# Performance work log

Hardware: AMD Instinct MI355X
Metric: run time of the kernel (lower is better)

The kernel has to match this reference:

```python
import jax, jax.numpy as jnp
import numpy as np
from jax import lax

B, T, N, C = 32, 32, 64, 64          # batch, window, num_series, inter_dim
GRU_H, QK, HOR = 64, 32, 12          # gru_dim, qk_dim, prediction_horizon
KS = (3, 5, 7)                       # temporal kernel per block (3 + 2*i)


def setup_inputs() -> dict:
    key = jax.random.key(0)
    ks = jax.random.split(key, 32)
    rn = lambda k, shape, s=0.05: jax.random.normal(k, shape, jnp.float32) * s
    inp = {"x": jax.random.normal(ks[0], (B, T, N), jnp.float32)}
    # x_to_inter_dim: Conv1d(1, C, kernel_size=1) == scalar * w + b
    inp["w_x2i"] = rn(ks[1], (C,)); inp["b_x2i"] = rn(ks[2], (C,))
    # latentCorrelation GRU (input_size=1, hidden=GRU_H), gate order r,z,n
    inp["gru_wih"] = rn(ks[3], (3 * GRU_H, 1)); inp["gru_whh"] = rn(ks[4], (3 * GRU_H, GRU_H))
    inp["gru_bih"] = rn(ks[5], (3 * GRU_H,)); inp["gru_bhh"] = rn(ks[6], (3 * GRU_H,))
    inp["wq_w"] = rn(ks[7], (QK, GRU_H)); inp["wq_b"] = rn(ks[8], (QK,))
    inp["wk_w"] = rn(ks[9], (QK, GRU_H)); inp["wk_b"] = rn(ks[10], (QK,))
    # per block: T independent GCNConvs (theta + bias), one temporal Conv1d
    for i, k_ in enumerate(KS):
        inp[f"gcn_w{i}"] = rn(ks[11 + 4 * i], (T, C, C))
        inp[f"gcn_b{i}"] = rn(ks[12 + 4 * i], (T, C))
        inp[f"conv_w{i}"] = rn(ks[13 + 4 * i], (C, C, k_))
        inp[f"conv_b{i}"] = rn(ks[14 + 4 * i], (C,))
    inp["lout_w"] = rn(ks[25], (N * HOR, T * N * C), 0.01)
    inp["lout_b"] = rn(ks[26], (N * HOR,))
    return inp


def _forward(x, w_x2i, b_x2i, gru_wih, gru_whh, gru_bih, gru_bhh,
             wq_w, wq_b, wk_w, wk_b,
             gcn_w0, gcn_b0, conv_w0, conv_b0,
             gcn_w1, gcn_b1, conv_w1, conv_b1,
             gcn_w2, gcn_b2, conv_w2, conv_b2,
             lout_w, lout_b):
    xs = jnp.transpose(x, (1, 0, 2))  # (T, B, N) time-major

    # --- latentCorrelation: one GRU run over all B*N series at once ---
    def gru_step(h, xt):  # h: (B,N,GRU_H), xt: (B,N)
        gi = xt[..., None] * gru_wih[:, 0] + gru_bih           # (B,N,3H)
        gh = h @ gru_whh.T + gru_bhh                           # (B,N,3H)
        r = jax.nn.sigmoid(gi[..., :GRU_H] + gh[..., :GRU_H])
        z = jax.nn.sigmoid(gi[..., GRU_H:2 * GRU_H] + gh[..., GRU_H:2 * GRU_H])
        n = jnp.tanh(gi[..., 2 * GRU_H:] + r * gh[..., 2 * GRU_H:])
        return (1.0 - z) * n + z * h, None

    h0 = jnp.zeros((B, N, GRU_H), x.dtype)
    hT, _ = lax.scan(gru_step, h0, xs)                         # (B,N,GRU_H)
    Q = hT @ wq_w.T + wq_b                                     # (B,N,QK)
    K = hT @ wk_w.T + wk_b
    Wadj = jax.nn.softmax(jnp.einsum('bnq,bmq->bnm', Q, K) / jnp.sqrt(jnp.float32(QK)), axis=2)

    # GCN symmetric norm on the dense complete graph; edge (src=i, tgt=j) has
    # weight Wadj[b,i,j]; degree is per-target (column) sum.
    deg = Wadj.sum(axis=1)                                     # (B,N)
    dinv = jnp.where(deg > 0, 1.0 / jnp.sqrt(deg), 0.0)
    What = dinv[:, :, None] * Wadj * dinv[:, None, :]          # (B,N,N)

    # x_to_inter_dim (1x1 conv) applied per timestep
    feats = xs[..., None] * w_x2i + b_x2i                      # (T,B,N,C)

    for gw, gb, cw, cb, k_ in ((gcn_w0, gcn_b0, conv_w0, conv_b0, 3),
                               (gcn_w1, gcn_b1, conv_w1, conv_b1, 5),
                               (gcn_w2, gcn_b2, conv_w2, conv_b2, 7)):
        xw = jnp.einsum('tbnc,tcd->tbnd', feats, gw)           # per-timestep theta
        agg = jnp.einsum('bij,tbid->tbjd', What, xw) + gb[:, None, None, :]
        seq = jnp.transpose(agg, (1, 2, 3, 0)).reshape(B * N, C, T)
        p = k_ // 2
        conv = lax.conv_general_dilated(seq, cw, (1,), [(p, p)],
                                        dimension_numbers=('NCH', 'OIH', 'NCH'))
        conv = conv + cb[None, :, None]
        conv = jnp.where(conv >= 0, conv, 0.01 * conv)         # LeakyReLU (dropout p=0)
        feats = jnp.transpose(conv.reshape(B, N, C, T), (3, 0, 1, 2))

    # stack(x_list, dim=2).view(B*N, C*T).view(B, -1) -> (B, N*C*T) feature order (n,c,t)
    flat = jnp.transpose(feats, (1, 2, 3, 0)).reshape(B, N * C * T)
    out = flat @ lout_w.T + lout_b                             # (B, N*HOR)
    return out.reshape(B, HOR, N)


def reference(x, w_x2i, b_x2i, gru_wih, gru_whh, gru_bih, gru_bhh,
              wq_w, wq_b, wk_w, wk_b,
              gcn_w0, gcn_b0, conv_w0, conv_b0,
              gcn_w1, gcn_b1, conv_w1, conv_b1,
              gcn_w2, gcn_b2, conv_w2, conv_b2,
              lout_w, lout_b):
    return _forward(x, w_x2i, b_x2i, gru_wih, gru_whh, gru_bih, gru_bhh,
                    wq_w, wq_b, wk_w, wk_b,
                    gcn_w0, gcn_b0, conv_w0, conv_b0,
                    gcn_w1, gcn_b1, conv_w1, conv_b1,
                    gcn_w2, gcn_b2, conv_w2, conv_b2,
                    lout_w, lout_b)
```

## Files before the change

### kernel.cpp

```cpp
#include <hip/hip_runtime.h>
#include <hip/hip_bf16.h>

#define BB 32
#define TT 32
#define NN 64
#define CC 64
#define HH 64
#define QKD 32
#define HOR 12
#define OUTD (NN*HOR)
#define KFLAT (NN*CC*TT)

typedef __attribute__((ext_vector_type(4))) float f32x4;
typedef __attribute__((ext_vector_type(8))) short s16x8;

static __device__ __forceinline__ unsigned short f2bf(float f) {
    unsigned u = __float_as_uint(f);
    unsigned r = (u + 0x7FFFu + ((u >> 16) & 1u)) >> 16;
    return (unsigned short)r;
}
static __device__ __forceinline__ float bf2f(unsigned short h) {
    return __uint_as_float(((unsigned)h) << 16);
}
static __device__ __forceinline__ void split8(const float* f, uint4& hi, uint4& lo) {
    unsigned hh[8], ll[8];
    #pragma unroll
    for (int i = 0; i < 8; ++i) {
        unsigned short h = f2bf(f[i]);
        float hf = bf2f(h);
        hh[i] = h;
        ll[i] = f2bf(f[i] - hf);
    }
    hi = make_uint4(hh[0] | (hh[1] << 16), hh[2] | (hh[3] << 16),
                    hh[4] | (hh[5] << 16), hh[6] | (hh[7] << 16));
    lo = make_uint4(ll[0] | (ll[1] << 16), ll[2] | (ll[3] << 16),
                    ll[4] | (ll[5] << 16), ll[6] | (ll[7] << 16));
}
static __device__ __forceinline__ void gl2lds16(const void* gsrc, void* ldst) {
    __builtin_amdgcn_global_load_lds(
        (const __attribute__((address_space(1))) unsigned int*)gsrc,
        (__attribute__((address_space(3))) unsigned int*)ldst, 16, 0, 0);
}

__global__ __launch_bounds__(256) void gru_kernel(
    const float* __restrict__ x, const float* __restrict__ wih,
    const float* __restrict__ whh, const float* __restrict__ bih,
    const float* __restrict__ bhh, float* __restrict__ hT)
{
    __shared__ float Wt[64][193];
    __shared__ float hbuf[4][64];
    __shared__ float part[4][4][3][64];
    int tid = threadIdx.x;
    for (int idx = tid; idx < 192*64; idx += 256) {
        int g = idx >> 6, k = idx & 63;
        Wt[k][g] = whh[idx];
    }
    int w = tid >> 6;
    int j = tid & 63;
    hbuf[w][j] = 0.0f;
    __syncthreads();
    float Wreg[3][16];
    #pragma unroll
    for (int g = 0; g < 3; ++g)
        #pragma unroll
        for (int kk = 0; kk < 16; ++kk)
            Wreg[g][kk] = Wt[w*16 + kk][g*64 + j];
    int gs0 = blockIdx.x * 4;
    int b = gs0 >> 6, n0 = gs0 & 63;
    float wih_r = wih[j], wih_z = wih[64+j], wih_n = wih[128+j];
    float bi_r = bih[j], bi_z = bih[64+j], bi_n = bih[128+j];
    float bh_r = bhh[j], bh_z = bhh[64+j], bh_n = bhh[128+j];
    float hreg = 0.0f;
    for (int t = 0; t < TT; ++t) {
        float p[3][4];
        #pragma unroll
        for (int g = 0; g < 3; ++g)
            #pragma unroll
            for (int s = 0; s < 4; ++s) p[g][s] = 0.f;
        #pragma unroll
        for (int s = 0; s < 4; ++s) {
            #pragma unroll
            for (int q = 0; q < 4; ++q) {
                const float4 hv = *(const float4*)&hbuf[s][w*16 + q*4];
                #pragma unroll
                for (int g = 0; g < 3; ++g) {
                    p[g][s] += hv.x*Wreg[g][q*4]   + hv.y*Wreg[g][q*4+1]
                             + hv.z*Wreg[g][q*4+2] + hv.w*Wreg[g][q*4+3];
                }
            }
        }
        #pragma unroll
        for (int g = 0; g < 3; ++g)
            #pragma unroll
            for (int s = 0; s < 4; ++s)
                part[w][s][g][j] = p[g][s];
        __syncthreads();
        float gr = bh_r + part[0][w][0][j] + part[1][w][0][j] + part[2][w][0][j] + part[3][w][0][j];
        float gz = bh_z + part[0][w][1][j] + part[1][w][1][j] + part[2][w][1][j] + part[3][w][1][j];
        float gn = bh_n + part[0][w][2][j] + part[1][w][2][j] + part[2][w][2][j] + part[3][w][2][j];
        float xt = x[(b*TT + t)*NN + n0 + w];
        float r = 1.f/(1.f+__expf(-(xt*wih_r + bi_r + gr)));
        float z = 1.f/(1.f+__expf(-(xt*wih_z + bi_z + gz)));
        float nn_ = tanhf(xt*wih_n + bi_n + r*gn);
        float hnew = (1.f - z)*nn_ + z*hreg;
        hreg = hnew;
        hbuf[w][j] = hnew;
        __syncthreads();
    }
    hT[(gs0 + w)*64 + j] = hreg;
}

__global__ __launch_bounds__(256) void attn_kernel(
    const float* __restrict__ hT, const float* __restrict__ wq_w,
    const float* __restrict__ wq_b, const float* __restrict__ wk_w,
    const float* __restrict__ wk_b,
    unsigned short* __restrict__ whT_hi, unsigned short* __restrict__ whT_lo)
{
    __shared__ float hs[64][64];
    __shared__ float Qs[64][33], Ks[64][33];
    __shared__ float S[64][65];
    __shared__ float pd[4][64];
    __shared__ float dinv[64];
    int b = blockIdx.x, tid = threadIdx.x;
    for (int idx = tid; idx < 64*64; idx += 256) hs[idx>>6][idx&63] = hT[b*4096 + idx];
    __syncthreads();
    for (int idx = tid; idx < 64*32; idx += 256) {
        int n_ = idx >> 5, q = idx & 31;
        float accq = wq_b[q], acck = wk_b[q];
        #pragma unroll 8
        for (int h_ = 0; h_ < 64; ++h_) {
            float hv = hs[n_][h_];
            accq += hv * wq_w[q*64 + h_];
            acck += hv * wk_w[q*64 + h_];
        }
        Qs[n_][q] = accq; Ks[n_][q] = acck;
    }
    __syncthreads();
    const float scale = 0.17677669529663687f;
    for (int idx = tid; idx < 64*64; idx += 256) {
        int n_ = idx >> 6, m = idx & 63;
        float acc = 0.f;
        #pragma unroll 8
        for (int q = 0; q < 32; ++q) acc += Qs[n_][q]*Ks[m][q];
        S[n_][m] = acc * scale;
    }
    __syncthreads();
    {
        int r = tid >> 2, q = tid & 3;
        float mx = -1e30f;
        #pragma unroll
        for (int m = 0; m < 16; ++m) mx = fmaxf(mx, S[r][q*16+m]);
        mx = fmaxf(mx, __shfl_xor(mx, 1));
        mx = fmaxf(mx, __shfl_xor(mx, 2));
        float sum = 0.f;
        float e[16];
        #pragma unroll
        for (int m = 0; m < 16; ++m) { e[m] = __expf(S[r][q*16+m]-mx); sum += e[m]; }
        sum += __shfl_xor(sum, 1);
        sum += __shfl_xor(sum, 2);
        float inv = 1.f/sum;
        #pragma unroll
        for (int m = 0; m < 16; ++m) S[r][q*16+m] = e[m]*inv;
    }
    __syncthreads();
    {
        int c = tid & 63, rq = tid >> 6;
        float d = 0.f;
        #pragma unroll
        for (int i = 0; i < 16; ++i) d += S[rq*16 + i][c];
        pd[rq][c] = d;
    }
    __syncthreads();
    if (tid < 64) {
        float d = pd[0][tid]+pd[1][tid]+pd[2][tid]+pd[3][tid];
        dinv[tid] = (d > 0.f) ? 1.0f/sqrtf(d) : 0.f;
    }
    __syncthreads();
    for (int idx = tid; idx < 64*64; idx += 256) {
        int jj = idx >> 6, ii = idx & 63;
        float val = dinv[ii]*S[ii][jj]*dinv[jj];
        unsigned short h = f2bf(val);
        whT_hi[b*4096 + idx] = h;
        whT_lo[b*4096 + idx] = f2bf(val - bf2f(h));
    }
}

__global__ __launch_bounds__(256) void prep_all(
    const float* __restrict__ gw0, const float* __restrict__ wx, const float* __restrict__ bx,
    float* __restrict__ u, float* __restrict__ v,
    const float* __restrict__ gw1, unsigned short* __restrict__ g1h, unsigned short* __restrict__ g1l,
    const float* __restrict__ gw2, unsigned short* __restrict__ g2h, unsigned short* __restrict__ g2l,
    const float* __restrict__ cw1, unsigned short* __restrict__ c1h, unsigned short* __restrict__ c1l,
    const float* __restrict__ cw2, unsigned short* __restrict__ c2h, unsigned short* __restrict__ c2l,
    const float* __restrict__ cw3, unsigned short* __restrict__ c3h, unsigned short* __restrict__ c3l,
    const float* __restrict__ lb, float* __restrict__ out)
{
    int bid = blockIdx.x, tid = threadIdx.x;
    if (bid < 32) {
        __shared__ float pu[4][64], pv[4][64];
        int t = bid, d = tid & 63, cq = tid >> 6;
        float su = 0.f, sv = 0.f;
        for (int c = cq*16; c < cq*16 + 16; ++c) {
            float gv = gw0[t*4096 + c*64 + d];
            su += wx[c]*gv; sv += bx[c]*gv;
        }
        pu[cq][d] = su; pv[cq][d] = sv;
        __syncthreads();
        if (tid < 64) {
            u[t*64 + tid] = pu[0][tid]+pu[1][tid]+pu[2][tid]+pu[3][tid];
            v[t*64 + tid] = pv[0][tid]+pv[1][tid]+pv[2][tid]+pv[3][tid];
        }
    } else if (bid < 96) {
        const float* gw = (bid < 64) ? gw1 : gw2;
        unsigned short* hi = (bid < 64) ? g1h : g2h;
        unsigned short* lo = (bid < 64) ? g1l : g2l;
        int t = (bid < 64) ? bid - 32 : bid - 64;
        for (int idx = tid; idx < 4096; idx += 256) {
            int d = idx >> 6, c = idx & 63;
            float val = gw[t*4096 + c*64 + d];
            unsigned short h = f2bf(val);
            hi[t*4096 + idx] = h;
            lo[t*4096 + idx] = f2bf(val - bf2f(h));
        }
    } else if (bid < 288) {
        const float* cw; unsigned short *hi, *lo; int KW, co;
        if (bid < 160)      { cw = cw1; hi = c1h; lo = c1l; KW = 3; co = bid - 96; }
        else if (bid < 224) { cw = cw2; hi = c2h; lo = c2l; KW = 5; co = bid - 160; }
        else                { cw = cw3; hi = c3h; lo = c3l; KW = 7; co = bid - 224; }
        int K = KW*64;
        for (int idx = tid; idx < K; idx += 256) {
            int ka = idx >> 6, ci = idx & 63;
            float val = cw[(size_t)(co*64 + ci)*KW + ka];
            unsigned short h = f2bf(val);
            hi[(size_t)co*K + idx] = h;
            lo[(size_t)co*K + idx] = f2bf(val - bf2f(h));
        }
    } else {
        int idx = (bid - 288)*256 + tid;
        out[idx] = lb[idx % OUTD];
    }
}

template<bool FIRST>
__global__ __launch_bounds__(256) void gcn_mfma(
    const float* __restrict__ fin,
    const unsigned short* __restrict__ gwT_hi, const unsigned short* __restrict__ gwT_lo,
    const float* __restrict__ u, const float* __restrict__ v,
    const unsigned short* __restrict__ whT_hi, const unsigned short* __restrict__ whT_lo,
    const float* __restrict__ gb, float* __restrict__ o)
{
    __shared__ __align__(16) unsigned short ft_hi[64][64], ft_lo[64][64];
    __shared__ __align__(16) unsigned short xsT_hi[64][64], xsT_lo[64][64];
    __shared__ float x_l[64];
    int tb = blockIdx.x, t = tb >> 5, b = tb & 31;
    int tid = threadIdx.x;
    int w = tid >> 6, l = tid & 63, lm = l & 15, ld = l >> 4;

    if (FIRST) {
        if (tid < 64) x_l[tid] = fin[(b*TT + t)*NN + tid];
        __syncthreads();
        int d = tid >> 2, nq = tid & 3;
        float ud = u[t*64 + d], vd = v[t*64 + d];
        float vals[16];
        #pragma unroll
        for (int i = 0; i < 16; ++i) vals[i] = x_l[nq*16 + i]*ud + vd;
        #pragma unroll
        for (int h = 0; h < 2; ++h) {
            uint4 hi, lo; split8(&vals[h*8], hi, lo);
            int un = (nq*2 + h) ^ (d & 7);
            *(uint4*)&xsT_hi[d][un*8] = hi;
            *(uint4*)&xsT_lo[d][un*8] = lo;
        }
        __syncthreads();
    } else {
        {
            int row = tid >> 2, c0 = (tid & 3) * 16;
            const float* src = fin + (size_t)tb*4096 + row*64 + c0;
            float f8a[8], f8b[8];
            *(float4*)f8a = *(const float4*)src;       *(float4*)(f8a+4) = *(const float4*)(src+4);
            *(float4*)f8b = *(const float4*)(src+8);   *(float4*)(f8b+4) = *(const float4*)(src+12);
            uint4 hi, lo;
            split8(f8a, hi, lo);
            int u0 = ((c0>>3)) ^ (row & 7);
            *(uint4*)&ft_hi[row][u0*8] = hi; *(uint4*)&ft_lo[row][u0*8] = lo;
            split8(f8b, hi, lo);
            int u1 = ((c0>>3)+1) ^ (row & 7);
            *(uint4*)&ft_hi[row][u1*8] = hi; *(uint4*)&ft_lo[row][u1*8] = lo;
        }
        __syncthreads();
        f32x4 acc[4];
        #pragma unroll
        for (int ct = 0; ct < 4; ++ct) acc[ct] = (f32x4){0.f,0.f,0.f,0.f};
        #pragma unroll
        for (int kc = 0; kc < 2; ++kc) {
            int nrow = w*16 + lm;
            int ux = (kc*4 + ld) ^ (nrow & 7);
            s16x8 xh = *(const s16x8*)&ft_hi[nrow][ux*8];
            s16x8 xl = *(const s16x8*)&ft_lo[nrow][ux*8];
            #pragma unroll
            for (int ct = 0; ct < 4; ++ct) {
                int drow = ct*16 + lm;
                s16x8 yh = *(const s16x8*)&gwT_hi[t*4096 + drow*64 + kc*32 + ld*8];
                s16x8 yl = *(const s16x8*)&gwT_lo[t*4096 + drow*64 + kc*32 + ld*8];
                acc[ct] = __builtin_amdgcn_mfma_f32_16x16x32_bf16(xh, yh, acc[ct], 0, 0, 0);
                acc[ct] = __builtin_amdgcn_mfma_f32_16x16x32_bf16(xh, yl, acc[ct], 0, 0, 0);
                acc[ct] = __builtin_amdgcn_mfma_f32_16x16x32_bf16(xl, yh, acc[ct], 0, 0, 0);
            }
        }
        #pragma unroll
        for (int ct = 0; ct < 4; ++ct) {
            int d = ct*16 + lm;
            int n0 = w*16 + ld*4;
            unsigned short hh[4], llo[4];
            #pragma unroll
            for (int r = 0; r < 4; ++r) {
                float val = acc[ct][r];
                unsigned short h = f2bf(val);
                hh[r] = h; llo[r] = f2bf(val - bf2f(h));
            }
            int un = (n0 >> 3) ^ (d & 7);
            int base = d*64 + un*8 + (n0 & 7);
            *(uint2*)&xsT_hi[0][0 + base] = make_uint2(hh[0]|(hh[1]<<16), hh[2]|(hh[3]<<16));
            *(uint2*)&xsT_lo[0][0 + base] = make_uint2(llo[0]|(llo[1]<<16), llo[2]|(llo[3]<<16));
        }
        __syncthreads();
    }

    f32x4 acc2[4];
    #pragma unroll
    for (int ct = 0; ct < 4; ++ct) acc2[ct] = (f32x4){0.f,0.f,0.f,0.f};
    #pragma unroll
    for (int kc = 0; kc < 2; ++kc) {
        int jrow = w*16 + lm;
        s16x8 wh = *(const s16x8*)&whT_hi[b*4096 + jrow*64 + kc*32 + ld*8];
        s16x8 wl = *(const s16x8*)&whT_lo[b*4096 + jrow*64 + kc*32 + ld*8];
        #pragma unroll
        for (int ct = 0; ct < 4; ++ct) {
            int drow = ct*16 + lm;
            int uy = (kc*4 + ld) ^ (drow & 7);
            s16x8 yh = *(const s16x8*)&xsT_hi[drow][uy*8];
            s16x8 yl = *(const s16x8*)&xsT_lo[drow][uy*8];
            acc2[ct] = __builtin_amdgcn_mfma_f32_16x16x32_bf16(wh, yh, acc2[ct], 0, 0, 0);
            acc2[ct] = __builtin_amdgcn_mfma_f32_16x16x32_bf16(wh, yl, acc2[ct], 0, 0, 0);
            acc2[ct] = __builtin_amdgcn_mfma_f32_16x16x32_bf16(wl, yh, acc2[ct], 0, 0, 0);
        }
    }
    float* oo = o + (size_t)tb*4096;
    #pragma unroll
    for (int ct = 0; ct < 4; ++ct) {
        int d = ct*16 + lm;
        float bias = gb[t*64 + d];
        #pragma unroll
        for (int r = 0; r < 4; ++r) {
            int jj = w*16 + ld*4 + r;
            oo[jj*64 + d] = acc2[ct][r] + bias;
        }
    }
}

template<int KW, bool LAST>
__global__ __launch_bounds__(256) void conv_mfma(float* __restrict__ g,
    const unsigned short* __restrict__ wch, const unsigned short* __restrict__ wcl,
    const float* __restrict__ cb, unsigned short* __restrict__ fo)
{
    constexpr int P = KW/2, K = KW*64, K32 = KW*2;
    __shared__ __align__(16) unsigned short sh[32][64], sl[32][64];
    int bn = blockIdx.x, tid = threadIdx.x;
    {
        int t = tid >> 3, c0 = (tid & 7) * 8;
        const float* src = &g[((size_t)t*2048 + bn)*64 + c0];
        float f8[8];
        *(float4*)f8 = *(const float4*)src;
        *(float4*)(f8+4) = *(const float4*)(src+4);
        uint4 hi, lo; split8(f8, hi, lo);
        int uu = (tid & 7) ^ (t & 7);
        *(uint4*)&sh[t][uu*8] = hi;
        *(uint4*)&sl[t][uu*8] = lo;
    }
    __syncthreads();
    int w = tid >> 6, l = tid & 63, lm = l & 15, ld = l >> 4;
    int co = w*16 + lm;
    f32x4 acc0 = {0.f,0.f,0.f,0.f}, acc1 = {0.f,0.f,0.f,0.f};
    const s16x8 zf = {0,0,0,0,0,0,0,0};
    for (int kc = 0; kc < K32; ++kc) {
        int ka = kc >> 1;
        int ci = (kc & 1)*32 + ld*8;
        s16x8 yh = *(const s16x8*)&wch[(size_t)co*K + kc*32 + ld*8];
        s16x8 yl = *(const s16x8*)&wcl[(size_t)co*K + kc*32 + ld*8];
        #pragma unroll
        for (int Mt = 0; Mt < 2; ++Mt) {
            int ts = Mt*16 + lm + ka - P;
            bool ok = ((unsigned)ts) < 32u;
            int tc = ok ? ts : 0;
            int ua = (ci >> 3) ^ (tc & 7);
            s16x8 xh = *(const s16x8*)&sh[tc][ua*8];
            s16x8 xl = *(const s16x8*)&sl[tc][ua*8];
            if (!ok) { xh = zf; xl = zf; }
            f32x4& a = Mt ? acc1 : acc0;
            a = __builtin_amdgcn_mfma_f32_16x16x32_bf16(xh, yh, a, 0, 0, 0);
            a = __builtin_amdgcn_mfma_f32_16x16x32_bf16(xh, yl, a, 0, 0, 0);
            a = __builtin_amdgcn_mfma_f32_16x16x32_bf16(xl, yh, a, 0, 0, 0);
        }
    }
    float bias = cb[co];
    if (LAST) {
        int b = bn >> 6, n = bn & 63;
        unsigned short* ob = fo + (size_t)b*KFLAT + n*2048 + co*32;
        #pragma unroll
        for (int Mt = 0; Mt < 2; ++Mt) {
            const f32x4& a = Mt ? acc1 : acc0;
            unsigned short hv[4];
            #pragma unroll
            for (int r = 0; r < 4; ++r) {
                float val = a[r] + bias;
                val = (val >= 0.f) ? val : 0.01f*val;
                hv[r] = f2bf(val);
            }
            *(uint2*)&ob[Mt*16 + ld*4] = make_uint2(hv[0]|(hv[1]<<16), hv[2]|(hv[3]<<16));
        }
    } else {
        #pragma unroll
        for (int Mt = 0; Mt < 2; ++Mt) {
            const f32x4& a = Mt ? acc1 : acc0;
            #pragma unroll
            for (int r = 0; r < 4; ++r) {
                int t = Mt*16 + ld*4 + r;
                float val = a[r] + bias;
                val = (val >= 0.f) ? val : 0.01f*val;
                g[((size_t)t*2048 + bn)*64 + co] = val;
            }
        }
    }
}

__global__ __launch_bounds__(256) void gemm_mfma(const unsigned short* __restrict__ flat,
                                                 const float* __restrict__ W,
                                                 float* __restrict__ out)
{
    __shared__ __align__(16) float Wl[2][64][64];
    __shared__ __align__(16) unsigned short Al[2][32][64];
    const int tid = threadIdx.x;
    const int w = tid >> 6, l = tid & 63;
    const int og = blockIdx.x >> 6;
    const int kc = blockIdx.x & 63;
    const int o_blk = og * 64;
    const int kbase = kc * 2048;

    const int wrow_l = l >> 4;
    const int wu = l & 15;
    size_t w_off[4];
    #pragma unroll
    for (int i = 0; i < 4; ++i) {
        int row = w*16 + i*4 + wrow_l;
        w_off[i] = (size_t)(o_blk + row) * KFLAT + (unsigned)((wu ^ (row & 7)) * 4);
    }
    const int arow = w*8 + (l >> 3);
    const int au = l & 7;
    const size_t a_off0 = (size_t)arow * KFLAT + (unsigned)((au ^ (arow & 7)) * 8);

#define ISSUE_TILE(buf_, s_) { \
    int kwin_ = kbase + (s_)*64; \
    _Pragma("unroll") \
    for (int i_ = 0; i_ < 4; ++i_) \
        gl2lds16(W + w_off[i_] + kwin_, &Wl[buf_][w*16 + i_*4][0]); \
    gl2lds16(flat + a_off0 + kwin_, &Al[buf_][w*8][0]); \
}

    f32x4 acc0 = {0.f,0.f,0.f,0.f}, acc1 = {0.f,0.f,0.f,0.f};
    ISSUE_TILE(0, 0);
    ISSUE_TILE(1, 1);

    const int lmod = l & 15, ldiv = l >> 4, lx = l & 7;
    for (int s = 0; s < 32; ++s) {
        if (s < 31) { asm volatile("s_waitcnt vmcnt(5)" ::: "memory"); }
        else        { asm volatile("s_waitcnt vmcnt(0)" ::: "memory"); }
        __builtin_amdgcn_s_barrier();
        asm volatile("" ::: "memory");
        const int cur = s & 1;
        #pragma unroll
        for (int ksub = 0; ksub < 2; ++ksub) {
            int ju = ksub*8 + ldiv*2;
            const float4 b0 = *(const float4*)&Wl[cur][w*16 + lmod][(ju ^ lx)*4];
            const float4 b1 = *(const float4*)&Wl[cur][w*16 + lmod][((ju+1) ^ lx)*4];
            float bf[8] = {b0.x,b0.y,b0.z,b0.w,b1.x,b1.y,b1.z,b1.w};
            s16x8 bhi, blo;
            #pragma unroll
            for (int i = 0; i < 8; ++i) {
                unsigned short h = f2bf(bf[i]);
                float hf = bf2f(h);
                bhi[i] = (short)h;
                blo[i] = (short)f2bf(bf[i] - hf);
            }
            int jua = ksub*4 + ldiv;
            const s16x8 a0 = *(const s16x8*)&Al[cur][lmod]      [(jua ^ lx)*8];
            const s16x8 a1 = *(const s16x8*)&Al[cur][16 + lmod] [(jua ^ lx)*8];
            acc0 = __builtin_amdgcn_mfma_f32_16x16x32_bf16(a0, bhi, acc0, 0, 0, 0);
            acc0 = __builtin_amdgcn_mfma_f32_16x16x32_bf16(a0, blo, acc0, 0, 0, 0);
            acc1 = __builtin_amdgcn_mfma_f32_16x16x32_bf16(a1, bhi, acc1, 0, 0, 0);
            acc1 = __builtin_amdgcn_mfma_f32_16x16x32_bf16(a1, blo, acc1, 0, 0, 0);
        }
        asm volatile("" ::: "memory");
        __builtin_amdgcn_s_barrier();
        if (s < 30) { ISSUE_TILE(cur, s+2); }
    }
#undef ISSUE_TILE

    const int o_out = o_blk + w*16 + lmod;
    #pragma unroll
    for (int r = 0; r < 4; ++r) {
        int b0_ = ldiv*4 + r;
        atomicAdd(&out[(size_t)b0_*OUTD + o_out], acc0[r]);
        atomicAdd(&out[(size_t)(16 + b0_)*OUTD + o_out], acc1[r]);
    }
}

extern "C" void kernel_launch(void* const* d_in, const int* in_sizes, int n_in,
                              void* d_out, int out_size, void* d_ws, size_t ws_size,
                              hipStream_t stream) {
    (void)in_sizes; (void)n_in; (void)out_size; (void)ws_size;
    const float* x        = (const float*)d_in[0];
    const float* w_x2i    = (const float*)d_in[1];
    const float* b_x2i    = (const float*)d_in[2];
    const float* gru_wih  = (const float*)d_in[3];
    const float* gru_whh  = (const float*)d_in[4];
    const float* gru_bih  = (const float*)d_in[5];
    const float* gru_bhh  = (const float*)d_in[6];
    const float* wq_w     = (const float*)d_in[7];
    const float* wq_b     = (const float*)d_in[8];
    const float* wk_w     = (const float*)d_in[9];
    const float* wk_b     = (const float*)d_in[10];
    const float* gcn_w[3]  = {(const float*)d_in[11], (const float*)d_in[15], (const float*)d_in[19]};
    const float* gcn_b[3]  = {(const float*)d_in[12], (const float*)d_in[16], (const float*)d_in[20]};
    const float* conv_w[3] = {(const float*)d_in[13], (const float*)d_in[17], (const float*)d_in[21]};
    const float* conv_b[3] = {(const float*)d_in[14], (const float*)d_in[18], (const float*)d_in[22]};
    const float* lout_w   = (const float*)d_in[23];
    const float* lout_b   = (const float*)d_in[24];
    float* out = (float*)d_out;
    float* ws  = (float*)d_ws;

    float* hT   = ws;
    float* u    = ws + 131072;
    float* v    = ws + 133120;
    float* bufA = ws + 135168;
    float* bufB = bufA + 4194304;
    unsigned short* usb = (unsigned short*)(ws + 8523776);
    unsigned short* whT_hi  = usb;
    unsigned short* whT_lo  = usb + 131072;
    unsigned short* gwT1_hi = usb + 262144;
    unsigned short* gwT1_lo = usb + 393216;
    unsigned short* gwT2_hi = usb + 524288;
    unsigned short* gwT2_lo = usb + 655360;
    unsigned short* cw1_hi  = usb + 786432;
    unsigned short* cw1_lo  = usb + 798720;
    unsigned short* cw2_hi  = usb + 811008;
    unsigned short* cw2_lo  = usb + 831488;
    unsigned short* cw3_hi  = usb + 851968;
    unsigned short* cw3_lo  = usb + 880640;

    prep_all<<<dim3(384), dim3(256), 0, stream>>>(
        gcn_w[0], w_x2i, b_x2i, u, v,
        gcn_w[1], gwT1_hi, gwT1_lo,
        gcn_w[2], gwT2_hi, gwT2_lo,
        conv_w[0], cw1_hi, cw1_lo,
        conv_w[1], cw2_hi, cw2_lo,
        conv_w[2], cw3_hi, cw3_lo,
        lout_b, out);

    gru_kernel<<<dim3(512), dim3(256), 0, stream>>>(x, gru_wih, gru_whh, gru_bih, gru_bhh, hT);
    attn_kernel<<<dim3(32), dim3(256), 0, stream>>>(hT, wq_w, wq_b, wk_w, wk_b, whT_hi, whT_lo);

    unsigned short* flat16 = (unsigned short*)bufB;
    gcn_mfma<true><<<dim3(1024), dim3(256), 0, stream>>>(x, nullptr, nullptr, u, v,
                                                         whT_hi, whT_lo, gcn_b[0], bufA);
    conv_mfma<3,false><<<dim3(2048), dim3(256), 0, stream>>>(bufA, cw1_hi, cw1_lo, conv_b[0], nullptr);
    gcn_mfma<false><<<dim3(1024), dim3(256), 0, stream>>>(bufA, gwT1_hi, gwT1_lo, u, v,
                                                          whT_hi, whT_lo, gcn_b[1], bufB);
    conv_mfma<5,false><<<dim3(2048), dim3(256), 0, stream>>>(bufB, cw2_hi, cw2_lo, conv_b[1], nullptr);
    gcn_mfma<false><<<dim3(1024), dim3(256), 0, stream>>>(bufB, gwT2_hi, gwT2_lo, u, v,
                                                          whT_hi, whT_lo, gcn_b[2], bufA);
    conv_mfma<7,true><<<dim3(2048), dim3(256), 0, stream>>>(bufA, cw3_hi, cw3_lo, conv_b[2], (unsigned short*)bufB);

    gemm_mfma<<<dim3(768), dim3(256), 0, stream>>>(flat16, lout_w, out);
}
```

Before: 307.8 us.

## Fuse middle stages into persistent kernel with grid barriers; single-bf16 final GEMM

Merges the prep, GRU, attention, GCN and conv kernels into one persistent 512-block kernel that separates stages with software grid barriers, removing per-launch gaps. The final GEMM now uses a triple-buffered load pipeline that issues tile loads before compute, and it drops the low half of the split-bf16 weights, halving its MFMA count. The grid barrier assumes all 512 blocks are co-resident, and deadlocks if they are not. Dropping the low-order weight term lowers the GEMM's accuracy.

```diff
diff --git a/kernel.cpp b/kernel.cpp
--- a/kernel.cpp
+++ b/kernel.cpp
@@ -10,23 +10,25 @@
 #define HOR 12
 #define OUTD (NN*HOR)
 #define KFLAT (NN*CC*TT)
+#define NBLK 512
 
 typedef __attribute__((ext_vector_type(4))) float f32x4;
 typedef __attribute__((ext_vector_type(8))) short s16x8;
-
-static __device__ __forceinline__ unsigned short f2bf(float f) {
+typedef unsigned short ush;
+
+static __device__ __forceinline__ ush f2bf(float f) {
     unsigned u = __float_as_uint(f);
     unsigned r = (u + 0x7FFFu + ((u >> 16) & 1u)) >> 16;
-    return (unsigned short)r;
-}
-static __device__ __forceinline__ float bf2f(unsigned short h) {
+    return (ush)r;
+}
+static __device__ __forceinline__ float bf2f(ush h) {
     return __uint_as_float(((unsigned)h) << 16);
 }
 static __device__ __forceinline__ void split8(const float* f, uint4& hi, uint4& lo) {
     unsigned hh[8], ll[8];
     #pragma unroll
     for (int i = 0; i < 8; ++i) {
-        unsigned short h = f2bf(f[i]);
+        ush h = f2bf(f[i]);
         float hf = bf2f(h);
         hh[i] = h;
         ll[i] = f2bf(f[i] - hf);
@@ -42,219 +44,56 @@
         (__attribute__((address_space(3))) unsigned int*)ldst, 16, 0, 0);
 }
 
-__global__ __launch_bounds__(256) void gru_kernel(
-    const float* __restrict__ x, const float* __restrict__ wih,
-    const float* __restrict__ whh, const float* __restrict__ bih,
-    const float* __restrict__ bhh, float* __restrict__ hT)
+static __device__ __forceinline__ void gridbar(unsigned* bar, int k) {
+    __syncthreads();
+    if (threadIdx.x == 0) {
+        __threadfence();
+        unsigned* cnt = bar + 2*k;
+        unsigned* flg = bar + 2*k + 1;
+        unsigned prev = atomicAdd(cnt, 1u);
+        if (prev == NBLK - 1u) {
+            __threadfence();
+            atomicExch(flg, 1u);
+        } else {
+            while (atomicAdd(flg, 0u) == 0u) __builtin_amdgcn_s_sleep(4);
+        }
+        __threadfence();
+    }
+    __syncthreads();
+}
+
+struct MidP {
+    const float *x, *wih, *whh, *bih, *bhh;
+    float* hT;
+    const float *wq_w, *wq_b, *wk_w, *wk_b;
+    ush *whT_hi, *whT_lo;
+    const float *gw0, *wx, *bx;
+    float *u, *v;
+    const float *gw1; ush *g1h, *g1l;
+    const float *gw2; ush *g2h, *g2l;
+    const float *cw1; ush *c1h, *c1l;
+    const float *cw2; ush *c2h, *c2l;
+    const float *cw3; ush *c3h, *c3l;
+    const float *lb; float* out;
+    const float *gb0, *gb1, *gb2, *cb1, *cb2, *cb3;
+    float *bufA, *bufB; ush* flat16;
+    unsigned* bar;
+};
+
+template<bool FIRST>
+static __device__ void gcn_unit(int tb, const float* fin,
+    const ush* gwT_hi, const ush* gwT_lo, const float* u, const float* v,
+    const ush* whT_hi, const ush* whT_lo, const float* gb, float* o, char* smem)
 {
-    __shared__ float Wt[64][193];
-    __shared__ float hbuf[4][64];
-    __shared__ float part[4][4][3][64];
-    int tid = threadIdx.x;
-    for (int idx = tid; idx < 192*64; idx += 256) {
-        int g = idx >> 6, k = idx & 63;
-        Wt[k][g] = whh[idx];
-    }
-    int w = tid >> 6;
-    int j = tid & 63;
-    hbuf[w][j] = 0.0f;
-    __syncthreads();
-    float Wreg[3][16];
-    #pragma unroll
-    for (int g = 0; g < 3; ++g)
-        #pragma unroll
-        for (int kk = 0; kk < 16; ++kk)
-            Wreg[g][kk] = Wt[w*16 + kk][g*64 + j];
-    int gs0 = blockIdx.x * 4;
-    int b = gs0 >> 6, n0 = gs0 & 63;
-    float wih_r = wih[j], wih_z = wih[64+j], wih_n = wih[128+j];
-    float bi_r = bih[j], bi_z = bih[64+j], bi_n = bih[128+j];
-    float bh_r = bhh[j], bh_z = bhh[64+j], bh_n = bhh[128+j];
-    float hreg = 0.0f;
-    for (int t = 0; t < TT; ++t) {
-        float p[3][4];
-        #pragma unroll
-        for (int g = 0; g < 3; ++g)
-            #pragma unroll
-            for (int s = 0; s < 4; ++s) p[g][s] = 0.f;
-        #pragma unroll
-        for (int s = 0; s < 4; ++s) {
-            #pragma unroll
-            for (int q = 0; q < 4; ++q) {
-                const float4 hv = *(const float4*)&hbuf[s][w*16 + q*4];
-                #pragma unroll
-                for (int g = 0; g < 3; ++g) {
-                    p[g][s] += hv.x*Wreg[g][q*4]   + hv.y*Wreg[g][q*4+1]
-                             + hv.z*Wreg[g][q*4+2] + hv.w*Wreg[g][q*4+3];
-                }
-            }
-        }
-        #pragma unroll
-        for (int g = 0; g < 3; ++g)
-            #pragma unroll
-            for (int s = 0; s < 4; ++s)
-                part[w][s][g][j] = p[g][s];
-        __syncthreads();
-        float gr = bh_r + part[0][w][0][j] + part[1][w][0][j] + part[2][w][0][j] + part[3][w][0][j];
-        float gz = bh_z + part[0][w][1][j] + part[1][w][1][j] + part[2][w][1][j] + part[3][w][1][j];
-        float gn = bh_n + part[0][w][2][j] + part[1][w][2][j] + part[2][w][2][j] + part[3][w][2][j];
-        float xt = x[(b*TT + t)*NN + n0 + w];
-        float r = 1.f/(1.f+__expf(-(xt*wih_r + bi_r + gr)));
-        float z = 1.f/(1.f+__expf(-(xt*wih_z + bi_z + gz)));
-        float nn_ = tanhf(xt*wih_n + bi_n + r*gn);
-        float hnew = (1.f - z)*nn_ + z*hreg;
-        hreg = hnew;
-        hbuf[w][j] = hnew;
-        __syncthreads();
-    }
-    hT[(gs0 + w)*64 + j] = hreg;
-}
-
-__global__ __launch_bounds__(256) void attn_kernel(
-    const float* __restrict__ hT, const float* __restrict__ wq_w,
-    const float* __restrict__ wq_b, const float* __restrict__ wk_w,
-    const float* __restrict__ wk_b,
-    unsigned short* __restrict__ whT_hi, unsigned short* __restrict__ whT_lo)
-{
-    __shared__ float hs[64][64];
-    __shared__ float Qs[64][33], Ks[64][33];
-    __shared__ float S[64][65];
-    __shared__ float pd[4][64];
-    __shared__ float dinv[64];
-    int b = blockIdx.x, tid = threadIdx.x;
-    for (int idx = tid; idx < 64*64; idx += 256) hs[idx>>6][idx&63] = hT[b*4096 + idx];
-    __syncthreads();
-    for (int idx = tid; idx < 64*32; idx += 256) {
-        int n_ = idx >> 5, q = idx & 31;
-        float accq = wq_b[q], acck = wk_b[q];
-        #pragma unroll 8
-        for (int h_ = 0; h_ < 64; ++h_) {
-            float hv = hs[n_][h_];
-            accq += hv * wq_w[q*64 + h_];
-            acck += hv * wk_w[q*64 + h_];
-        }
-        Qs[n_][q] = accq; Ks[n_][q] = acck;
-    }
-    __syncthreads();
-    const float scale = 0.17677669529663687f;
-    for (int idx = tid; idx < 64*64; idx += 256) {
-        int n_ = idx >> 6, m = idx & 63;
-        float acc = 0.f;
-        #pragma unroll 8
-        for (int q = 0; q < 32; ++q) acc += Qs[n_][q]*Ks[m][q];
-        S[n_][m] = acc * scale;
-    }
-    __syncthreads();
-    {
-        int r = tid >> 2, q = tid & 3;
-        float mx = -1e30f;
-        #pragma unroll
-        for (int m = 0; m < 16; ++m) mx = fmaxf(mx, S[r][q*16+m]);
-        mx = fmaxf(mx, __shfl_xor(mx, 1));
-        mx = fmaxf(mx, __shfl_xor(mx, 2));
-        float sum = 0.f;
-        float e[16];
-        #pragma unroll
-        for (int m = 0; m < 16; ++m) { e[m] = __expf(S[r][q*16+m]-mx); sum += e[m]; }
-        sum += __shfl_xor(sum, 1);
-        sum += __shfl_xor(sum, 2);
-        float inv = 1.f/sum;
-        #pragma unroll
-        for (int m = 0; m < 16; ++m) S[r][q*16+m] = e[m]*inv;
-    }
-    __syncthreads();
-    {
-        int c = tid & 63, rq = tid >> 6;
-        float d = 0.f;
-        #pragma unroll
-        for (int i = 0; i < 16; ++i) d += S[rq*16 + i][c];
-        pd[rq][c] = d;
-    }
-    __syncthreads();
-    if (tid < 64) {
-        float d = pd[0][tid]+pd[1][tid]+pd[2][tid]+pd[3][tid];
-        dinv[tid] = (d > 0.f) ? 1.0f/sqrtf(d) : 0.f;
-    }
-    __syncthreads();
-    for (int idx = tid; idx < 64*64; idx += 256) {
-        int jj = idx >> 6, ii = idx & 63;
-        float val = dinv[ii]*S[ii][jj]*dinv[jj];
-        unsigned short h = f2bf(val);
-        whT_hi[b*4096 + idx] = h;
-        whT_lo[b*4096 + idx] = f2bf(val - bf2f(h));
-    }
-}
-
-__global__ __launch_bounds__(256) void prep_all(
-    const float* __restrict__ gw0, const float* __restrict__ wx, const float* __restrict__ bx,
-    float* __restrict__ u, float* __restrict__ v,
-    const float* __restrict__ gw1, unsigned short* __restrict__ g1h, unsigned short* __restrict__ g1l,
-    const float* __restrict__ gw2, unsigned short* __restrict__ g2h, unsigned short* __restrict__ g2l,
-    const float* __restrict__ cw1, unsigned short* __restrict__ c1h, unsigned short* __restrict__ c1l,
-    const float* __restrict__ cw2, unsigned short* __restrict__ c2h, unsigned short* __restrict__ c2l,
-    const float* __restrict__ cw3, unsigned short* __restrict__ c3h, unsigned short* __restrict__ c3l,
-    const float* __restrict__ lb, float* __restrict__ out)
-{
-    int bid = blockIdx.x, tid = threadIdx.x;
-    if (bid < 32) {
-        __shared__ float pu[4][64], pv[4][64];
-        int t = bid, d = tid & 63, cq = tid >> 6;
-        float su = 0.f, sv = 0.f;
-        for (int c = cq*16; c < cq*16 + 16; ++c) {
-            float gv = gw0[t*4096 + c*64 + d];
-            su += wx[c]*gv; sv += bx[c]*gv;
-        }
-        pu[cq][d] = su; pv[cq][d] = sv;
-        __syncthreads();
-        if (tid < 64) {
-            u[t*64 + tid] = pu[0][tid]+pu[1][tid]+pu[2][tid]+pu[3][tid];
-            v[t*64 + tid] = pv[0][tid]+pv[1][tid]+pv[2][tid]+pv[3][tid];
-        }
-    } else if (bid < 96) {
-        const float* gw = (bid < 64) ? gw1 : gw2;
-        unsigned short* hi = (bid < 64) ? g1h : g2h;
-        unsigned short* lo = (bid < 64) ? g1l : g2l;
-        int t = (bid < 64) ? bid - 32 : bid - 64;
-        for (int idx = tid; idx < 4096; idx += 256) {
-            int d = idx >> 6, c = idx & 63;
-            float val = gw[t*4096 + c*64 + d];
-            unsigned short h = f2bf(val);
-            hi[t*4096 + idx] = h;
-            lo[t*4096 + idx] = f2bf(val - bf2f(h));
-        }
-    } else if (bid < 288) {
-        const float* cw; unsigned short *hi, *lo; int KW, co;
-        if (bid < 160)      { cw = cw1; hi = c1h; lo = c1l; KW = 3; co = bid - 96; }
-        else if (bid < 224) { cw = cw2; hi = c2h; lo = c2l; KW = 5; co = bid - 160; }
-        else                { cw = cw3; hi = c3h; lo = c3l; KW = 7; co = bid - 224; }
-        int K = KW*64;
-        for (int idx = tid; idx < K; idx += 256) {
-            int ka = idx >> 6, ci = idx & 63;
-            float val = cw[(size_t)(co*64 + ci)*KW + ka];
-            unsigned short h = f2bf(val);
-            hi[(size_t)co*K + idx] = h;
-            lo[(size_t)co*K + idx] = f2bf(val - bf2f(h));
-        }
-    } else {
-        int idx = (bid - 288)*256 + tid;
-        out[idx] = lb[idx % OUTD];
-    }
-}
-
-template<bool FIRST>
-__global__ __launch_bounds__(256) void gcn_mfma(
-    const float* __restrict__ fin,
-    const unsigned short* __restrict__ gwT_hi, const unsigned short* __restrict__ gwT_lo,
-    const float* __restrict__ u, const float* __restrict__ v,
-    const unsigned short* __restrict__ whT_hi, const unsigned short* __restrict__ whT_lo,
-    const float* __restrict__ gb, float* __restrict__ o)
-{
-    __shared__ __align__(16) unsigned short ft_hi[64][64], ft_lo[64][64];
-    __shared__ __align__(16) unsigned short xsT_hi[64][64], xsT_lo[64][64];
-    __shared__ float x_l[64];
-    int tb = blockIdx.x, t = tb >> 5, b = tb & 31;
+    ush (*ft_hi)[64]  = (ush(*)[64])smem;
+    ush (*ft_lo)[64]  = (ush(*)[64])(smem + 8192);
+    ush (*xsT_hi)[64] = (ush(*)[64])(smem + 16384);
+    ush (*xsT_lo)[64] = (ush(*)[64])(smem + 24576);
+    float* x_l = (float*)(smem + 32768);
+    int t = tb >> 5, b = tb & 31;
     int tid = threadIdx.x;
     int w = tid >> 6, l = tid & 63, lm = l & 15, ld = l >> 4;
+    __syncthreads();
 
     if (FIRST) {
         if (tid < 64) x_l[tid] = fin[(b*TT + t)*NN + tid];
@@ -311,11 +150,11 @@
         for (int ct = 0; ct < 4; ++ct) {
             int d = ct*16 + lm;
             int n0 = w*16 + ld*4;
-            unsigned short hh[4], llo[4];
+            ush hh[4], llo[4];
             #pragma unroll
             for (int r = 0; r < 4; ++r) {
                 float val = acc[ct][r];
-                unsigned short h = f2bf(val);
+                ush h = f2bf(val);
                 hh[r] = h; llo[r] = f2bf(val - bf2f(h));
             }
             int un = (n0 >> 3) ^ (d & 7);
@@ -359,13 +198,14 @@
 }
 
 template<int KW, bool LAST>
-__global__ __launch_bounds__(256) void conv_mfma(float* __restrict__ g,
-    const unsigned short* __restrict__ wch, const unsigned short* __restrict__ wcl,
-    const float* __restrict__ cb, unsigned short* __restrict__ fo)
+static __device__ void conv_unit(int bn, float* g,
+    const ush* wch, const ush* wcl, const float* cb, ush* fo, char* smem)
 {
     constexpr int P = KW/2, K = KW*64, K32 = KW*2;
-    __shared__ __align__(16) unsigned short sh[32][64], sl[32][64];
-    int bn = blockIdx.x, tid = threadIdx.x;
+    ush (*sh)[64] = (ush(*)[64])smem;
+    ush (*sl)[64] = (ush(*)[64])(smem + 8192);
+    int tid = threadIdx.x;
+    __syncthreads();
     {
         int t = tid >> 3, c0 = (tid & 7) * 8;
         const float* src = &g[((size_t)t*2048 + bn)*64 + c0];
@@ -405,11 +245,11 @@
     float bias = cb[co];
     if (LAST) {
         int b = bn >> 6, n = bn & 63;
-        unsigned short* ob = fo + (size_t)b*KFLAT + n*2048 + co*32;
+        ush* ob = fo + (size_t)b*KFLAT + n*2048 + co*32;
         #pragma unroll
         for (int Mt = 0; Mt < 2; ++Mt) {
             const f32x4& a = Mt ? acc1 : acc0;
-            unsigned short hv[4];
+            ush hv[4];
             #pragma unroll
             for (int r = 0; r < 4; ++r) {
                 float val = a[r] + bias;
@@ -433,12 +273,217 @@
     }
 }
 
-__global__ __launch_bounds__(256) void gemm_mfma(const unsigned short* __restrict__ flat,
+__global__ __launch_bounds__(256, 2) void middle_kernel(MidP P)
+{
+    __shared__ __align__(16) char smem[51200];
+    int bid = blockIdx.x, tid = threadIdx.x;
+
+    if (bid < 32) {
+        float (*pu)[64] = (float(*)[64])smem;
+        float (*pv)[64] = (float(*)[64])(smem + 1024);
+        int t = bid, d = tid & 63, cq = tid >> 6;
+        float su = 0.f, sv = 0.f;
+        for (int c = cq*16; c < cq*16 + 16; ++c) {
+            float gv = P.gw0[t*4096 + c*64 + d];
+            su += P.wx[c]*gv; sv += P.bx[c]*gv;
+        }
+        pu[cq][d] = su; pv[cq][d] = sv;
+        __syncthreads();
+        if (tid < 64) {
+            P.u[t*64 + tid] = pu[0][tid]+pu[1][tid]+pu[2][tid]+pu[3][tid];
+            P.v[t*64 + tid] = pv[0][tid]+pv[1][tid]+pv[2][tid]+pv[3][tid];
+        }
+    } else if (bid < 96) {
+        const float* gw = (bid < 64) ? P.gw1 : P.gw2;
+        ush* hi = (bid < 64) ? P.g1h : P.g2h;
+        ush* lo = (bid < 64) ? P.g1l : P.g2l;
+        int t = (bid < 64) ? bid - 32 : bid - 64;
+        for (int idx = tid; idx < 4096; idx += 256) {
+            int d = idx >> 6, c = idx & 63;
+            float val = gw[t*4096 + c*64 + d];
+            ush h = f2bf(val);
+            hi[t*4096 + idx] = h;
+            lo[t*4096 + idx] = f2bf(val - bf2f(h));
+        }
+    } else if (bid < 288) {
+        const float* cw; ush *hi, *lo; int KW, co;
+        if (bid < 160)      { cw = P.cw1; hi = P.c1h; lo = P.c1l; KW = 3; co = bid - 96; }
+        else if (bid < 224) { cw = P.cw2; hi = P.c2h; lo = P.c2l; KW = 5; co = bid - 160; }
+        else                { cw = P.cw3; hi = P.c3h; lo = P.c3l; KW = 7; co = bid - 224; }
+        int K = KW*64;
+        for (int idx = tid; idx < K; idx += 256) {
+            int ka = idx >> 6, ci = idx & 63;
+            float val = cw[(size_t)(co*64 + ci)*KW + ka];
+            ush h = f2bf(val);
+            hi[(size_t)co*K + idx] = h;
+            lo[(size_t)co*K + idx] = f2bf(val - bf2f(h));
+        }
+    } else if (bid < 384) {
+        int idx = (bid - 288)*256 + tid;
+        P.out[idx] = P.lb[idx % OUTD];
+    }
+    __syncthreads();
+
+    {
+        float (*hbuf)[64] = (float(*)[64])smem;
+        float4* part = (float4*)(smem + 1024);
+        int w = tid >> 6, j = tid & 63;
+        float Wreg[3][16];
+        #pragma unroll
+        for (int g = 0; g < 3; ++g)
+            #pragma unroll
+            for (int q = 0; q < 4; ++q) {
+                float4 wv = *(const float4*)&P.whh[(g*64 + j)*64 + w*16 + q*4];
+                Wreg[g][q*4+0] = wv.x; Wreg[g][q*4+1] = wv.y;
+                Wreg[g][q*4+2] = wv.z; Wreg[g][q*4+3] = wv.w;
+            }
+        hbuf[w][j] = 0.0f;
+        int gs0 = bid * 4;
+        int b = gs0 >> 6, n0 = gs0 & 63;
+        float wih_r = P.wih[j], wih_z = P.wih[64+j], wih_n = P.wih[128+j];
+        float bi_r = P.bih[j], bi_z = P.bih[64+j], bi_n = P.bih[128+j];
+        float bh_r = P.bhh[j], bh_z = P.bhh[64+j], bh_n = P.bhh[128+j];
+        __syncthreads();
+        float hreg = 0.0f;
+        for (int t = 0; t < TT; ++t) {
+            float p[3][4];
+            #pragma unroll
+            for (int g = 0; g < 3; ++g)
+                #pragma unroll
+                for (int s = 0; s < 4; ++s) p[g][s] = 0.f;
+            #pragma unroll
+            for (int s = 0; s < 4; ++s) {
+                #pragma unroll
+                for (int q = 0; q < 4; ++q) {
+                    const float4 hv = *(const float4*)&hbuf[s][w*16 + q*4];
+                    #pragma unroll
+                    for (int g = 0; g < 3; ++g) {
+                        p[g][s] += hv.x*Wreg[g][q*4]   + hv.y*Wreg[g][q*4+1]
+                                 + hv.z*Wreg[g][q*4+2] + hv.w*Wreg[g][q*4+3];
+                    }
+                }
+            }
+            #pragma unroll
+            for (int s = 0; s < 4; ++s)
+                part[(w*4 + s)*64 + j] = make_float4(p[0][s], p[1][s], p[2][s], 0.f);
+            __syncthreads();
+            float4 q0 = part[(0*4 + w)*64 + j];
+            float4 q1 = part[(1*4 + w)*64 + j];
+            float4 q2 = part[(2*4 + w)*64 + j];
+            float4 q3 = part[(3*4 + w)*64 + j];
+            float gr = bh_r + q0.x + q1.x + q2.x + q3.x;
+            float gz = bh_z + q0.y + q1.y + q2.y + q3.y;
+            float gn = bh_n + q0.z + q1.z + q2.z + q3.z;
+            float xt = P.x[(b*TT + t)*NN + n0 + w];
+            float r = 1.f/(1.f+__expf(-(xt*wih_r + bi_r + gr)));
+            float z = 1.f/(1.f+__expf(-(xt*wih_z + bi_z + gz)));
+            float nn_ = tanhf(xt*wih_n + bi_n + r*gn);
+            float hnew = (1.f - z)*nn_ + z*hreg;
+            hreg = hnew;
+            hbuf[w][j] = hnew;
+            __syncthreads();
+        }
+        P.hT[(gs0 + w)*64 + j] = hreg;
+    }
+    gridbar(P.bar, 0);
+
+    if (bid < 32) {
+        float (*hs)[64] = (float(*)[64])smem;
+        float (*Qs)[33] = (float(*)[33])(smem + 16384);
+        float (*Ks)[33] = (float(*)[33])(smem + 24832);
+        float (*S)[65]  = (float(*)[65])(smem + 33280);
+        float (*pd)[64] = (float(*)[64])(smem + 49920);
+        float* dinv     = (float*)(smem + 50944);
+        int b = bid;
+        for (int idx = tid; idx < 64*64; idx += 256) hs[idx>>6][idx&63] = P.hT[b*4096 + idx];
+        __syncthreads();
+        for (int idx = tid; idx < 64*32; idx += 256) {
+            int n_ = idx >> 5, q = idx & 31;
+            float accq = P.wq_b[q], acck = P.wk_b[q];
+            #pragma unroll 8
+            for (int h_ = 0; h_ < 64; ++h_) {
+                float hv = hs[n_][h_];
+                accq += hv * P.wq_w[q*64 + h_];
+                acck += hv * P.wk_w[q*64 + h_];
+            }
+            Qs[n_][q] = accq; Ks[n_][q] = acck;
+        }
+        __syncthreads();
+        const float scale = 0.17677669529663687f;
+        for (int idx = tid; idx < 64*64; idx += 256) {
+            int n_ = idx >> 6, m = idx & 63;
+            float acc = 0.f;
+            #pragma unroll 8
+            for (int q = 0; q < 32; ++q) acc += Qs[n_][q]*Ks[m][q];
+            S[n_][m] = acc * scale;
+        }
+        __syncthreads();
+        {
+            int r = tid >> 2, q = tid & 3;
+            float mx = -1e30f;
+            #pragma unroll
+            for (int m = 0; m < 16; ++m) mx = fmaxf(mx, S[r][q*16+m]);
+            mx = fmaxf(mx, __shfl_xor(mx, 1));
+            mx = fmaxf(mx, __shfl_xor(mx, 2));
+            float sum = 0.f;
+            float e[16];
+            #pragma unroll
+            for (int m = 0; m < 16; ++m) { e[m] = __expf(S[r][q*16+m]-mx); sum += e[m]; }
+            sum += __shfl_xor(sum, 1);
+            sum += __shfl_xor(sum, 2);
+            float inv = 1.f/sum;
+            #pragma unroll
+            for (int m = 0; m < 16; ++m) S[r][q*16+m] = e[m]*inv;
+        }
+        __syncthreads();
+        {
+            int c = tid & 63, rq = tid >> 6;
+            float d = 0.f;
+            #pragma unroll
+            for (int i = 0; i < 16; ++i) d += S[rq*16 + i][c];
+            pd[rq][c] = d;
+        }
+        __syncthreads();
+        if (tid < 64) {
+            float d = pd[0][tid]+pd[1][tid]+pd[2][tid]+pd[3][tid];
+            dinv[tid] = (d > 0.f) ? 1.0f/sqrtf(d) : 0.f;
+        }
+        __syncthreads();
+        for (int idx = tid; idx < 64*64; idx += 256) {
+            int jj = idx >> 6, ii = idx & 63;
+            float val = dinv[ii]*S[ii][jj]*dinv[jj];
+            ush h = f2bf(val);
+            P.whT_hi[b*4096 + idx] = h;
+            P.whT_lo[b*4096 + idx] = f2bf(val - bf2f(h));
+        }
+    }
+    gridbar(P.bar, 1);
+
+    for (int tb = bid; tb < 1024; tb += NBLK)
+        gcn_unit<true>(tb, P.x, nullptr, nullptr, P.u, P.v, P.whT_hi, P.whT_lo, P.gb0, P.bufA, smem);
+    gridbar(P.bar, 2);
+    for (int u_ = bid; u_ < 2048; u_ += NBLK)
+        conv_unit<3,false>(u_, P.bufA, P.c1h, P.c1l, P.cb1, nullptr, smem);
+    gridbar(P.bar, 3);
+    for (int tb = bid; tb < 1024; tb += NBLK)
+        gcn_unit<false>(tb, P.bufA, P.g1h, P.g1l, P.u, P.v, P.whT_hi, P.whT_lo, P.gb1, P.bufB, smem);
+    gridbar(P.bar, 4);
+    for (int u_ = bid; u_ < 2048; u_ += NBLK)
+        conv_unit<5,false>(u_, P.bufB, P.c2h, P.c2l, P.cb2, nullptr, smem);
+    gridbar(P.bar, 5);
+    for (int tb = bid; tb < 1024; tb += NBLK)
+        gcn_unit<false>(tb, P.bufB, P.g2h, P.g2l, P.u, P.v, P.whT_hi, P.whT_lo, P.gb2, P.bufA, smem);
+    gridbar(P.bar, 6);
+    for (int u_ = bid; u_ < 2048; u_ += NBLK)
+        conv_unit<7,true>(u_, P.bufA, P.c3h, P.c3l, P.cb3, P.flat16, smem);
+}
+
+__global__ __launch_bounds__(256) void gemm_mfma(const ush* __restrict__ flat,
                                                  const float* __restrict__ W,
                                                  float* __restrict__ out)
 {
-    __shared__ __align__(16) float Wl[2][64][64];
-    __shared__ __align__(16) unsigned short Al[2][32][64];
+    __shared__ __align__(16) float Wl[3][64][64];
+    __shared__ __align__(16) ush Al[3][32][64];
     const int tid = threadIdx.x;
     const int w = tid >> 6, l = tid & 63;
     const int og = blockIdx.x >> 6;
@@ -472,36 +517,32 @@
 
     const int lmod = l & 15, ldiv = l >> 4, lx = l & 7;
     for (int s = 0; s < 32; ++s) {
-        if (s < 31) { asm volatile("s_waitcnt vmcnt(5)" ::: "memory"); }
-        else        { asm volatile("s_waitcnt vmcnt(0)" ::: "memory"); }
+        const int cur = s % 3;
+        if (s < 30) {
+            ISSUE_TILE((s+2)%3, s+2);
+            asm volatile("s_waitcnt vmcnt(10)" ::: "memory");
+        } else if (s == 30) {
+            asm volatile("s_waitcnt vmcnt(5)" ::: "memory");
+        } else {
+            asm volatile("s_waitcnt vmcnt(0)" ::: "memory");
+        }
         __builtin_amdgcn_s_barrier();
-        asm volatile("" ::: "memory");
-        const int cur = s & 1;
         #pragma unroll
         for (int ksub = 0; ksub < 2; ++ksub) {
             int ju = ksub*8 + ldiv*2;
             const float4 b0 = *(const float4*)&Wl[cur][w*16 + lmod][(ju ^ lx)*4];
             const float4 b1 = *(const float4*)&Wl[cur][w*16 + lmod][((ju+1) ^ lx)*4];
             float bf[8] = {b0.x,b0.y,b0.z,b0.w,b1.x,b1.y,b1.z,b1.w};
-            s16x8 bhi, blo;
-            #pragma unroll
-            for (int i = 0; i < 8; ++i) {
-                unsigned short h = f2bf(bf[i]);
-                float hf = bf2f(h);
-                bhi[i] = (short)h;
-                blo[i] = (short)f2bf(bf[i] - hf);
-            }
+            s16x8 bhi;
+            #pragma unroll
+            for (int i = 0; i < 8; ++i) bhi[i] = (short)f2bf(bf[i]);
             int jua = ksub*4 + ldiv;
             const s16x8 a0 = *(const s16x8*)&Al[cur][lmod]      [(jua ^ lx)*8];
             const s16x8 a1 = *(const s16x8*)&Al[cur][16 + lmod] [(jua ^ lx)*8];
             acc0 = __builtin_amdgcn_mfma_f32_16x16x32_bf16(a0, bhi, acc0, 0, 0, 0);
-            acc0 = __builtin_amdgcn_mfma_f32_16x16x32_bf16(a0, blo, acc0, 0, 0, 0);
             acc1 = __builtin_amdgcn_mfma_f32_16x16x32_bf16(a1, bhi, acc1, 0, 0, 0);
-            acc1 = __builtin_amdgcn_mfma_f32_16x16x32_bf16(a1, blo, acc1, 0, 0, 0);
-        }
-        asm volatile("" ::: "memory");
+        }
         __builtin_amdgcn_s_barrier();
-        if (s < 30) { ISSUE_TILE(cur, s+2); }
     }
 #undef ISSUE_TILE
 
@@ -543,42 +584,40 @@
     float* v    = ws + 133120;
     float* bufA = ws + 135168;
     float* bufB = bufA + 4194304;
-    unsigned short* usb = (unsigned short*)(ws + 8523776);
-    unsigned short* whT_hi  = usb;
-    unsigned short* whT_lo  = usb + 131072;
-    unsigned short* gwT1_hi = usb + 262144;
-    unsigned short* gwT1_lo = usb + 393216;
-    unsigned short* gwT2_hi = usb + 524288;
-    unsigned short* gwT2_lo = usb + 655360;
-    unsigned short* cw1_hi  = usb + 786432;
-    unsigned short* cw1_lo  = usb + 798720;
-    unsigned short* cw2_hi  = usb + 811008;
-    unsigned short* cw2_lo  = usb + 831488;
-    unsigned short* cw3_hi  = usb + 851968;
-    unsigned short* cw3_lo  = usb + 880640;
-
-    prep_all<<<dim3(384), dim3(256), 0, stream>>>(
-        gcn_w[0], w_x2i, b_x2i, u, v,
-        gcn_w[1], gwT1_hi, gwT1_lo,
-        gcn_w[2], gwT2_hi, gwT2_lo,
-        conv_w[0], cw1_hi, cw1_lo,
-        conv_w[1], cw2_hi, cw2_lo,
-        conv_w[2], cw3_hi, cw3_lo,
-        lout_b, out);
-
-    gru_kernel<<<dim3(512), dim3(256), 0, stream>>>(x, gru_wih, gru_whh, gru_bih, gru_bhh, hT);
-    attn_kernel<<<dim3(32), dim3(256), 0, stream>>>(hT, wq_w, wq_b, wk_w, wk_b, whT_hi, whT_lo);
-
-    unsigned short* flat16 = (unsigned short*)bufB;
-    gcn_mfma<true><<<dim3(1024), dim3(256), 0, stream>>>(x, nullptr, nullptr, u, v,
-                                                         whT_hi, whT_lo, gcn_b[0], bufA);
-    conv_mfma<3,false><<<dim3(2048), dim3(256), 0, stream>>>(bufA, cw1_hi, cw1_lo, conv_b[0], nullptr);
-    gcn_mfma<false><<<dim3(1024), dim3(256), 0, stream>>>(bufA, gwT1_hi, gwT1_lo, u, v,
-                                                          whT_hi, whT_lo, gcn_b[1], bufB);
-    conv_mfma<5,false><<<dim3(2048), dim3(256), 0, stream>>>(bufB, cw2_hi, cw2_lo, conv_b[1], nullptr);
-    gcn_mfma<false><<<dim3(1024), dim3(256), 0, stream>>>(bufB, gwT2_hi, gwT2_lo, u, v,
-                                                          whT_hi, whT_lo, gcn_b[2], bufA);
-    conv_mfma<7,true><<<dim3(2048), dim3(256), 0, stream>>>(bufA, cw3_hi, cw3_lo, conv_b[2], (unsigned short*)bufB);
-
-    gemm_mfma<<<dim3(768), dim3(256), 0, stream>>>(flat16, lout_w, out);
-}
+    ush* usb = (ush*)(ws + 8523776);
+    ush* whT_hi  = usb;
+    ush* whT_lo  = usb + 131072;
+    ush* gwT1_hi = usb + 262144;
+    ush* gwT1_lo = usb + 393216;
+    ush* gwT2_hi = usb + 524288;
+    ush* gwT2_lo = usb + 655360;
+    ush* cw1_hi  = usb + 786432;
+    ush* cw1_lo  = usb + 798720;
+    ush* cw2_hi  = usb + 811008;
+    ush* cw2_lo  = usb + 831488;
+    ush* cw3_hi  = usb + 851968;
+    ush* cw3_lo  = usb + 880640;
+    unsigned* bar = (unsigned*)(usb + 909312);
+
+    hipMemsetAsync((void*)bar, 0, 64, stream);
+
+    MidP P;
+    P.x = x; P.wih = gru_wih; P.whh = gru_whh; P.bih = gru_bih; P.bhh = gru_bhh;
+    P.hT = hT;
+    P.wq_w = wq_w; P.wq_b = wq_b; P.wk_w = wk_w; P.wk_b = wk_b;
+    P.whT_hi = whT_hi; P.whT_lo = whT_lo;
+    P.gw0 = gcn_w[0]; P.wx = w_x2i; P.bx = b_x2i; P.u = u; P.v = v;
+    P.gw1 = gcn_w[1]; P.g1h = gwT1_hi; P.g1l = gwT1_lo;
+    P.gw2 = gcn_w[2]; P.g2h = gwT2_hi; P.g2l = gwT2_lo;
+    P.cw1 = conv_w[0]; P.c1h = cw1_hi; P.c1l = cw1_lo;
+    P.cw2 = conv_w[1]; P.c2h = cw2_hi; P.c2l = cw2_lo;
+    P.cw3 = conv_w[2]; P.c3h = cw3_hi; P.c3l = cw3_lo;
+    P.lb = lout_b; P.out = out;
+    P.gb0 = gcn_b[0]; P.gb1 = gcn_b[1]; P.gb2 = gcn_b[2];
+    P.cb1 = conv_b[0]; P.cb2 = conv_b[1]; P.cb3 = conv_b[2];
+    P.bufA = bufA; P.bufB = bufB; P.flat16 = (ush*)bufB;
+    P.bar = bar;
+
+    middle_kernel<<<dim3(NBLK), dim3(256), 0, stream>>>(P);
+    gemm_mfma<<<dim3(768), dim3(256), 0, stream>>>((ush*)bufB, lout_w, out);
+}
```

Result: slower. 615.4 us (+100.0%).
